# Kernel optimization log

Hardware: AMD Instinct MI355X
Metric: run time of the kernel (lower is better)

## Reference

```python
import jax, jax.numpy as jnp
import numpy as np

HEADS = 8
OUT_C = 8
NEG_SLOPE = 0.2  # PyG GATConv default


def setup_inputs() -> dict:
    key = jax.random.key(0)
    k = jax.random.split(key, 6)
    N, F, E = 100000, 128, 1600000
    x = jax.random.normal(k[0], (N, F), dtype=jnp.float32)
    edge_index = jax.random.randint(k[1], (2, E), 0, N, dtype=jnp.int64)
    W = jax.random.normal(k[2], (F, HEADS * OUT_C), dtype=jnp.float32) * (1.0 / np.sqrt(F))
    att_src = jax.random.normal(k[3], (HEADS, OUT_C), dtype=jnp.float32) * 0.1
    att_dst = jax.random.normal(k[4], (HEADS, OUT_C), dtype=jnp.float32) * 0.1
    bias = jnp.zeros((HEADS * OUT_C,), dtype=jnp.float32)
    return {"x": x, "edge_index": edge_index, "W": W,
            "att_src": att_src, "att_dst": att_dst, "bias": bias}


def reference(x, edge_index, W, att_src, att_dst, bias):
    N = x.shape[0]
    # add self loops (PyG default add_self_loops=True)
    loops = jnp.arange(N, dtype=edge_index.dtype)
    src = jnp.concatenate([edge_index[0], loops])  # [E']
    dst = jnp.concatenate([edge_index[1], loops])  # [E']

    h = (x @ W).reshape(N, HEADS, OUT_C)          # [N,H,C]
    a_src = jnp.einsum('nhc,hc->nh', h, att_src)  # [N,H]
    a_dst = jnp.einsum('nhc,hc->nh', h, att_dst)  # [N,H]

    # per-edge LeakyReLU attention logits
    e = jax.nn.leaky_relu(a_src[src] + a_dst[dst], NEG_SLOPE)  # [E',H]

    # segment softmax over incoming edges of each destination node
    emax = jax.ops.segment_max(e, dst, num_segments=N)  # every node has a self loop
    ex = jnp.exp(e - emax[dst])
    denom = jax.ops.segment_sum(ex, dst, num_segments=N)
    alpha = ex / denom[dst]  # [E',H]  (dropout on alpha skipped: eval mode)

    # scatter-add weighted source features
    out = jax.ops.segment_sum(alpha[:, :, None] * h[src], dst, num_segments=N)  # [N,H,C]
    return out.reshape(N, HEADS * OUT_C) + bias
```

## Files before the change

### kernel.cpp

```cpp
#include <hip/hip_runtime.h>
#include <hip/hip_bf16.h>


#define F 128
#define HC 64
#define H 8
#define NS 32
#define PB 512

__device__ inline ushort f2bf(float f) {
    unsigned u = __float_as_uint(f);
    u += 0x7fff + ((u >> 16) & 1);
    return (ushort)(u >> 16);
}

__global__ __launch_bounds__(256) void k_gemm(const float* __restrict__ x,
                                              const float* __restrict__ W,
                                              const float* __restrict__ att_src,
                                              const float* __restrict__ att_dst,
                                              ushort* __restrict__ h2,
                                              float* __restrict__ a_src,
                                              float* __restrict__ a_dst, int N) {
    __shared__ float xs[64][F];
    const int tid  = threadIdx.x;
    const int row0 = blockIdx.x * 64;
    #pragma unroll
    for (int i = 0; i < 8; ++i) {
        int idx = i * 256 + tid;
        int r = idx >> 5;
        float4 v = make_float4(0.f, 0.f, 0.f, 0.f);
        if (row0 + r < N) v = ((const float4*)x)[(size_t)row0 * 32 + idx];
        ((float4*)xs)[idx] = v;
    }
    __syncthreads();
    const int c0 = (tid & 15) * 4;
    const int r0 = (tid >> 4) * 4;
    float acc[4][4] = {};
    for (int k = 0; k < F; k += 4) {
        float w[4][4];
        *(float4*)w[0] = *(const float4*)&W[(size_t)(k + 0) * HC + c0];
        *(float4*)w[1] = *(const float4*)&W[(size_t)(k + 1) * HC + c0];
        *(float4*)w[2] = *(const float4*)&W[(size_t)(k + 2) * HC + c0];
        *(float4*)w[3] = *(const float4*)&W[(size_t)(k + 3) * HC + c0];
        #pragma unroll
        for (int i = 0; i < 4; ++i) {
            float4 xv = *(const float4*)&xs[r0 + i][k];
            #pragma unroll
            for (int c = 0; c < 4; ++c) {
                acc[i][c] += xv.x * w[0][c];
                acc[i][c] += xv.y * w[1][c];
                acc[i][c] += xv.z * w[2][c];
                acc[i][c] += xv.w * w[3][c];
            }
        }
    }
    const int head = (tid & 15) >> 1;
    const int cb   = c0 & 7;
    float as4[4], ad4[4];
    #pragma unroll
    for (int c = 0; c < 4; ++c) {
        as4[c] = att_src[head * 8 + cb + c];
        ad4[c] = att_dst[head * 8 + cb + c];
    }
    #pragma unroll
    for (int i = 0; i < 4; ++i) {
        int r = row0 + r0 + i;
        if (r < N) {
            ushort4 pk;
            pk.x = f2bf(acc[i][0]); pk.y = f2bf(acc[i][1]);
            pk.z = f2bf(acc[i][2]); pk.w = f2bf(acc[i][3]);
            *(ushort4*)&h2[(size_t)r * HC + c0] = pk;
            float ps = acc[i][0]*as4[0] + acc[i][1]*as4[1] +
                       acc[i][2]*as4[2] + acc[i][3]*as4[3];
            float pd = acc[i][0]*ad4[0] + acc[i][1]*ad4[1] +
                       acc[i][2]*ad4[2] + acc[i][3]*ad4[3];
            ps += __shfl_xor(ps, 1);
            pd += __shfl_xor(pd, 1);
            if ((tid & 1) == 0) {
                a_src[(size_t)r * H + head] = ps;
                a_dst[(size_t)r * H + head] = pd;
            }
        }
    }
}

__device__ inline unsigned grp_of(int d, unsigned Mg) {
    return (unsigned)(((unsigned long long)(unsigned)d * Mg) >> 32);
}

__global__ __launch_bounds__(256) void k_c(const int* __restrict__ ei,
                                           int* __restrict__ pcntT,
                                           int E, unsigned Mg) {
    __shared__ int cnt[8];
    if (threadIdx.x < 8) cnt[threadIdx.x] = 0;
    __syncthreads();
    const int t    = blockIdx.x * 256 + threadIdx.x;
    const int nthr = PB * 256;
    const int a0 = (4 - (E & 3)) & 3;
    const int nv = (E - a0) >> 2;
    const int4* vd = (const int4*)(ei + E + a0);
    for (int q = t; q < nv; q += nthr) {
        int4 d = vd[q];
        atomicAdd(&cnt[grp_of(d.x, Mg)], 1);
        atomicAdd(&cnt[grp_of(d.y, Mg)], 1);
        atomicAdd(&cnt[grp_of(d.z, Mg)], 1);
        atomicAdd(&cnt[grp_of(d.w, Mg)], 1);
    }
    if (blockIdx.x == 0) {
        int r = (E - a0) & 3;
        int e = -1;
        int tx = (int)threadIdx.x;
        if (tx < a0) e = tx;
        else if (tx - a0 < r) e = a0 + (nv << 2) + (tx - a0);
        if (e >= 0) atomicAdd(&cnt[grp_of(ei[E + e], Mg)], 1);
    }
    __syncthreads();
    if (threadIdx.x < 8) pcntT[(size_t)threadIdx.x * PB + blockIdx.x] = cnt[threadIdx.x];
}

__global__ __launch_bounds__(1024) void k_sA(int* __restrict__ pcntT,
                                             int* __restrict__ gEdgeBase, int E) {
    __shared__ int s[1024];
    const int S2 = 8 * PB;
    const int base = threadIdx.x * (S2 / 1024);
    int v[4]; int sum = 0;
    #pragma unroll
    for (int k = 0; k < S2 / 1024; ++k) { v[k] = pcntT[base + k]; sum += v[k]; }
    s[threadIdx.x] = sum;
    __syncthreads();
    for (int d = 1; d < 1024; d <<= 1) {
        int t = (threadIdx.x >= d) ? s[threadIdx.x - d] : 0;
        __syncthreads();
        s[threadIdx.x] += t;
        __syncthreads();
    }
    int run = s[threadIdx.x] - sum;
    #pragma unroll
    for (int k = 0; k < S2 / 1024; ++k) {
        int idx = base + k;
        pcntT[idx] = run;
        if ((idx % PB) == 0) gEdgeBase[idx / PB] = run;
        run += v[k];
    }
    if (threadIdx.x == 0) gEdgeBase[8] = E;
}

__global__ __launch_bounds__(256) void k_p(const int* __restrict__ ei,
                                           const int* __restrict__ pcntT,
                                           unsigned* __restrict__ payload,
                                           int E, unsigned Mg, int npg) {
    __shared__ int lpos[8];
    if (threadIdx.x < 8) lpos[threadIdx.x] = pcntT[(size_t)threadIdx.x * PB + blockIdx.x];
    __syncthreads();
    const int t    = blockIdx.x * 256 + threadIdx.x;
    const int nthr = PB * 256;
    const int a0 = (4 - (E & 3)) & 3;
    const int nv = (E - a0) >> 2;
    const int4* vd = (const int4*)(ei + E + a0);
    for (int q = t; q < nv; q += nthr) {
        int4 d = vd[q];
        int e = a0 + (q << 2);
        int s0 = ei[e], s1 = ei[e + 1], s2 = ei[e + 2], s3 = ei[e + 3];
        unsigned g; int pos;
        g = grp_of(d.x, Mg); pos = atomicAdd(&lpos[g], 1);
        payload[pos] = ((unsigned)s0 << 14) | (unsigned)(d.x - (int)g * npg);
        g = grp_of(d.y, Mg); pos = atomicAdd(&lpos[g], 1);
        payload[pos] = ((unsigned)s1 << 14) | (unsigned)(d.y - (int)g * npg);
        g = grp_of(d.z, Mg); pos = atomicAdd(&lpos[g], 1);
        payload[pos] = ((unsigned)s2 << 14) | (unsigned)(d.z - (int)g * npg);
        g = grp_of(d.w, Mg); pos = atomicAdd(&lpos[g], 1);
        payload[pos] = ((unsigned)s3 << 14) | (unsigned)(d.w - (int)g * npg);
    }
    if (blockIdx.x == 0) {
        int r = (E - a0) & 3;
        int e = -1;
        int tx = (int)threadIdx.x;
        if (tx < a0) e = tx;
        else if (tx - a0 < r) e = a0 + (nv << 2) + (tx - a0);
        if (e >= 0) {
            int dv = ei[E + e];
            unsigned g = grp_of(dv, Mg);
            int pos = atomicAdd(&lpos[g], 1);
            payload[pos] = ((unsigned)ei[e] << 14) | (unsigned)(dv - (int)g * npg);
        }
    }
}

__global__ __launch_bounds__(1024) void k_h2(const unsigned* __restrict__ payload,
                                             const int* __restrict__ gEdgeBase,
                                             ushort* __restrict__ hist, int npg) {
    extern __shared__ int lcnt[];
    const int g = blockIdx.x & 7, sl = blockIdx.x >> 3;
    for (int i = threadIdx.x; i < npg; i += 1024) lcnt[i] = 0;
    __syncthreads();
    const int gb0 = gEdgeBase[g], gb1 = gEdgeBase[g + 1];
    const int chunk = (gb1 - gb0 + NS - 1) / NS;
    const int lo = gb0 + sl * chunk;
    const int hi = min(lo + chunk, gb1);
    for (int i = lo + threadIdx.x; i < hi; i += 1024)
        atomicAdd(&lcnt[payload[i] & 16383u], 1);
    __syncthreads();
    ushort* hrow = hist + (size_t)blockIdx.x * npg;
    for (int i = threadIdx.x; i < npg; i += 1024) hrow[i] = (ushort)lcnt[i];
}

__global__ __launch_bounds__(256) void k_scan1(const ushort* __restrict__ hist,
                                               int* __restrict__ offs,
                                               int* __restrict__ bsums,
                                               int N, int npg) {
    __shared__ int s[256];
    int i = blockIdx.x * 256 + threadIdx.x;
    int v = 0;
    if (i < N) {
        int g = i / npg;
        int c = i - g * npg;
        const ushort* hp = hist + (size_t)g * npg + c;
        #pragma unroll 8
        for (int j = 0; j < NS; ++j) v += hp[(size_t)(j << 3) * npg];
        v += 1;
    }
    s[threadIdx.x] = v;
    __syncthreads();
    for (int d = 1; d < 256; d <<= 1) {
        int t = (threadIdx.x >= d) ? s[threadIdx.x - d] : 0;
        __syncthreads();
        s[threadIdx.x] += t;
        __syncthreads();
    }
    if (i < N) offs[i] = s[threadIdx.x] - v;
    if (threadIdx.x == 255) bsums[blockIdx.x] = s[255];
}

__global__ __launch_bounds__(512) void k_scan2(int* __restrict__ bsums, int nb) {
    __shared__ int s[512];
    int v = (threadIdx.x < nb) ? bsums[threadIdx.x] : 0;
    s[threadIdx.x] = v;
    __syncthreads();
    for (int d = 1; d < 512; d <<= 1) {
        int t = (threadIdx.x >= d) ? s[threadIdx.x - d] : 0;
        __syncthreads();
        s[threadIdx.x] += t;
        __syncthreads();
    }
    if (threadIdx.x < nb) bsums[threadIdx.x] = s[threadIdx.x] - v;
}

__global__ __launch_bounds__(256) void k_scan3(int* __restrict__ offs,
                                               const int* __restrict__ bsums,
                                               ushort* __restrict__ hist,
                                               int* __restrict__ srcs,
                                               int N, int npg, int Etot) {
    int i = blockIdx.x * 256 + threadIdx.x;
    if (i == 0) offs[N] = Etot;
    if (i >= N) return;
    int o = offs[i] + bsums[i >> 8];
    offs[i] = o;
    srcs[o] = i;
    int g = i / npg;
    int c = i - g * npg;
    ushort* hp = hist + (size_t)g * npg + c;
    int p = 0;
    #pragma unroll 8
    for (int j = 0; j < NS; ++j) {
        size_t off = (size_t)(j << 3) * npg;
        int t = hp[off];
        hp[off] = (ushort)p;
        p += t;
    }
}

__global__ __launch_bounds__(1024) void k_scat2(const unsigned* __restrict__ payload,
                                                const int* __restrict__ gEdgeBase,
                                                const ushort* __restrict__ hist,
                                                const int* __restrict__ offs,
                                                int* __restrict__ srcs,
                                                int npg, int N) {
    extern __shared__ int lpos[];
    const int g = blockIdx.x & 7, sl = blockIdx.x >> 3;
    const int lod = g * npg;
    const int len = min(npg, N - lod);
    const ushort* hrow = hist + (size_t)blockIdx.x * npg;
    for (int i = threadIdx.x; i < len; i += 1024)
        lpos[i] = offs[lod + i] + 1 + (int)hrow[i];
    __syncthreads();
    const int gb0 = gEdgeBase[g], gb1 = gEdgeBase[g + 1];
    const int chunk = (gb1 - gb0 + NS - 1) / NS;
    const int lo = gb0 + sl * chunk;
    const int hi = min(lo + chunk, gb1);
    for (int i = lo + threadIdx.x; i < hi; i += 1024) {
        unsigned p = payload[i];
        int pos = atomicAdd(&lpos[p & 16383u], 1);
        srcs[pos] = (int)(p >> 14);
    }
}

__global__ __launch_bounds__(256) void k_gat(const int* __restrict__ offs,
                                             const int* __restrict__ srcs,
                                             const ushort* __restrict__ h2,
                                             const float* __restrict__ a_src,
                                             const float* __restrict__ a_dst,
                                             const float* __restrict__ bias,
                                             float* __restrict__ out, int N) {
    const int lane = threadIdx.x & 63;
    const int half = lane >> 5;
    const int l32  = lane & 31;
    const int g    = l32 >> 3;
    const int hd   = l32 & 7;
    const int wave = threadIdx.x >> 6;
    const int d = blockIdx.x * 8 + wave * 2 + half;
    const bool valid = d < N;

    int off = 0, end = 0;
    float adst = 0.f;
    if (valid) {
        off  = offs[d];
        end  = offs[d + 1];
        adst = a_dst[d * H + hd];
    }

    float acc[8] = {0.f, 0.f, 0.f, 0.f, 0.f, 0.f, 0.f, 0.f};
    float den = 0.f;

    for (int i = off + g; i < end; i += 8) {
        const int i2 = i + 4;
        const bool has1 = (i2 < end);
        int s0 = srcs[i];
        int s1 = has1 ? srcs[i2] : s0;
        float a0 = a_src[s0 * H + hd] + adst;
        float a1 = a_src[s1 * H + hd] + adst;
        a0 = a0 > 0.f ? a0 : 0.2f * a0;
        a1 = a1 > 0.f ? a1 : 0.2f * a1;
        float ex0 = __expf(a0);
        float ex1 = has1 ? __expf(a1) : 0.f;
        uint4 u0 = *(const uint4*)(h2 + ((size_t)s0 << 6) + (hd << 3));
        uint4 u1 = *(const uint4*)(h2 + ((size_t)s1 << 6) + (hd << 3));
        acc[0] += ex0 * __uint_as_float(u0.x << 16);
        acc[1] += ex0 * __uint_as_float(u0.x & 0xffff0000u);
        acc[2] += ex0 * __uint_as_float(u0.y << 16);
        acc[3] += ex0 * __uint_as_float(u0.y & 0xffff0000u);
        acc[4] += ex0 * __uint_as_float(u0.z << 16);
        acc[5] += ex0 * __uint_as_float(u0.z & 0xffff0000u);
        acc[6] += ex0 * __uint_as_float(u0.w << 16);
        acc[7] += ex0 * __uint_as_float(u0.w & 0xffff0000u);
        acc[0] += ex1 * __uint_as_float(u1.x << 16);
        acc[1] += ex1 * __uint_as_float(u1.x & 0xffff0000u);
        acc[2] += ex1 * __uint_as_float(u1.y << 16);
        acc[3] += ex1 * __uint_as_float(u1.y & 0xffff0000u);
        acc[4] += ex1 * __uint_as_float(u1.z << 16);
        acc[5] += ex1 * __uint_as_float(u1.z & 0xffff0000u);
        acc[6] += ex1 * __uint_as_float(u1.w << 16);
        acc[7] += ex1 * __uint_as_float(u1.w & 0xffff0000u);
        den += ex0 + ex1;
    }

    #pragma unroll
    for (int m = 8; m <= 16; m <<= 1) {
        #pragma unroll
        for (int c = 0; c < 8; ++c) acc[c] += __shfl_xor(acc[c], m);
        den += __shfl_xor(den, m);
    }

    if (g == 0 && valid) {
        float r = 1.f / den;
        float4 o0, o1;
        o0.x = acc[0]*r + bias[hd*8+0]; o0.y = acc[1]*r + bias[hd*8+1];
        o0.z = acc[2]*r + bias[hd*8+2]; o0.w = acc[3]*r + bias[hd*8+3];
        o1.x = acc[4]*r + bias[hd*8+4]; o1.y = acc[5]*r + bias[hd*8+5];
        o1.z = acc[6]*r + bias[hd*8+6]; o1.w = acc[7]*r + bias[hd*8+7];
        *(float4*)&out[(size_t)d * HC + hd * 8]     = o0;
        *(float4*)&out[(size_t)d * HC + hd * 8 + 4] = o1;
    }
}

extern "C" void kernel_launch(void* const* d_in, const int* in_sizes, int n_in,
                              void* d_out, int out_size, void* d_ws, size_t ws_size,
                              hipStream_t stream) {
    const float* x       = (const float*)d_in[0];
    const int*   ei      = (const int*)d_in[1];
    const float* W       = (const float*)d_in[2];
    const float* att_src = (const float*)d_in[3];
    const float* att_dst = (const float*)d_in[4];
    const float* bias    = (const float*)d_in[5];
    const int N = in_sizes[0] / F;
    const int E = in_sizes[1] / 2;
    const int Etot = E + N;
    const int npg = (N + 7) / 8;
    const unsigned Mg = (unsigned)(((1ULL << 32) + (unsigned)npg - 1) / (unsigned)npg);
    float* out = (float*)d_out;

    ushort*   h2      = (ushort*)d_ws;
    float*    a_src   = (float*)(h2 + (size_t)N * HC);
    float*    a_dst   = a_src + (size_t)N * H;
    int*      offs    = (int*)(a_dst + (size_t)N * H);
    int*      bsums   = offs + N + 1;
    int*      pcntT   = bsums + 512;
    int*      gEdgeBase = pcntT + 8 * PB;
    ushort*   hist    = (ushort*)(gEdgeBase + 16);
    size_t    histE   = ((size_t)8 * NS * npg + 3) & ~(size_t)3;
    unsigned* payload = (unsigned*)(hist + histE);
    int*      srcs    = (int*)(payload + E);

    const int nb = (N + 255) / 256;
    const size_t ldsz = (size_t)npg * sizeof(int);
    k_gemm <<<(N + 63) / 64, 256, 0, stream>>>(x, W, att_src, att_dst, h2, a_src, a_dst, N);
    k_c    <<<PB, 256, 0, stream>>>(ei, pcntT, E, Mg);
    k_sA   <<<1, 1024, 0, stream>>>(pcntT, gEdgeBase, E);
    k_p    <<<PB, 256, 0, stream>>>(ei, pcntT, payload, E, Mg, npg);
    k_h2   <<<8 * NS, 1024, ldsz, stream>>>(payload, gEdgeBase, hist, npg);
    k_scan1<<<nb, 256, 0, stream>>>(hist, offs, bsums, N, npg);
    k_scan2<<<1, 512, 0, stream>>>(bsums, nb);
    k_scan3<<<nb, 256, 0, stream>>>(offs, bsums, hist, srcs, N, npg, Etot);
    k_scat2<<<8 * NS, 1024, ldsz, stream>>>(payload, gEdgeBase, hist, offs, srcs, npg, N);
    k_gat  <<<(N + 7) / 8, 256, 0, stream>>>(offs, srcs, h2, a_src, a_dst, bias, out, N);
}
```

Baseline: 224.2 us.

## Fuse edge counting into GEMM and merge scan stages into fewer kernels

Moves the per-block destination-group counting into the tail of the GEMM kernel, which runs with more than PB blocks. Each k_p block now redundantly scans the 4096 partial counts itself instead of relying on a separate single-block scan kernel. The three-kernel CSR offset scan is replaced by a reduce kernel plus a kernel that scans the block sums locally and then does the block scan and histogram rewrite. Together these cut the launch count from ten to seven, trading extra redundant scan work per block and extra register use (32 cached histogram values per thread).

Result: faster. 218.3 us (-2.6%).

```diff
diff --git a/kernel.cpp b/kernel.cpp
--- a/kernel.cpp
+++ b/kernel.cpp
@@ -5,6 +5,7 @@
 #define F 128
 #define HC 64
 #define H 8
+#define NG 8
 #define NS 32
 #define PB 512
 
@@ -12,6 +13,10 @@
     unsigned u = __float_as_uint(f);
     u += 0x7fff + ((u >> 16) & 1);
     return (ushort)(u >> 16);
+}
+
+__device__ inline unsigned grp_of(int d, unsigned Mg) {
+    return (unsigned)(((unsigned long long)(unsigned)d * Mg) >> 32);
 }
 
 __global__ __launch_bounds__(256) void k_gemm(const float* __restrict__ x,
@@ -20,8 +25,12 @@
                                               const float* __restrict__ att_dst,
                                               ushort* __restrict__ h2,
                                               float* __restrict__ a_src,
-                                              float* __restrict__ a_dst, int N) {
+                                              float* __restrict__ a_dst,
+                                              const int* __restrict__ ei,
+                                              int* __restrict__ pcntT,
+                                              int N, int E, unsigned Mg) {
     __shared__ float xs[64][F];
+    __shared__ int cnt8[8];
     const int tid  = threadIdx.x;
     const int row0 = blockIdx.x * 64;
     #pragma unroll
@@ -82,106 +91,92 @@
             }
         }
     }
-}
-
-__device__ inline unsigned grp_of(int d, unsigned Mg) {
-    return (unsigned)(((unsigned long long)(unsigned)d * Mg) >> 32);
-}
-
-__global__ __launch_bounds__(256) void k_c(const int* __restrict__ ei,
-                                           int* __restrict__ pcntT,
-                                           int E, unsigned Mg) {
-    __shared__ int cnt[8];
-    if (threadIdx.x < 8) cnt[threadIdx.x] = 0;
-    __syncthreads();
-    const int t    = blockIdx.x * 256 + threadIdx.x;
-    const int nthr = PB * 256;
+
+    if (blockIdx.x < PB) {
+        if (tid < 8) cnt8[tid] = 0;
+        __syncthreads();
+        const int a0 = (4 - (E & 3)) & 3;
+        const int nv = (E - a0) >> 2;
+        const int4* vd = (const int4*)(ei + E + a0);
+        for (int q = blockIdx.x * 256 + tid; q < nv; q += PB * 256) {
+            int4 d = vd[q];
+            atomicAdd(&cnt8[grp_of(d.x, Mg)], 1);
+            atomicAdd(&cnt8[grp_of(d.y, Mg)], 1);
+            atomicAdd(&cnt8[grp_of(d.z, Mg)], 1);
+            atomicAdd(&cnt8[grp_of(d.w, Mg)], 1);
+        }
+        if (blockIdx.x == 0) {
+            int r = (E - a0) & 3;
+            int e = -1;
+            if (tid < a0) e = tid;
+            else if (tid - a0 < r) e = a0 + (nv << 2) + (tid - a0);
+            if (e >= 0) atomicAdd(&cnt8[grp_of(ei[E + e], Mg)], 1);
+        }
+        __syncthreads();
+        if (tid < 8) pcntT[tid * PB + blockIdx.x] = cnt8[tid];
+    }
+}
+
+__global__ __launch_bounds__(256) void k_p(const int* __restrict__ ei,
+                                           const int* __restrict__ pcntT,
+                                           unsigned* __restrict__ payload,
+                                           int* __restrict__ gEdgeBase,
+                                           int E, unsigned Mg, int npg) {
+    __shared__ int sc[NG * PB];
+    __shared__ int sp[256];
+    __shared__ int cur[8];
+    const int tid = threadIdx.x;
+    for (int i = tid; i < NG * PB; i += 256) sc[i] = pcntT[i];
+    __syncthreads();
+    const int b16 = tid * 16;
+    int tmp[16]; int ssum = 0;
+    #pragma unroll
+    for (int k = 0; k < 16; ++k) { tmp[k] = sc[b16 + k]; ssum += tmp[k]; }
+    sp[tid] = ssum;
+    __syncthreads();
+    for (int d = 1; d < 256; d <<= 1) {
+        int t2 = (tid >= d) ? sp[tid - d] : 0;
+        __syncthreads();
+        sp[tid] += t2;
+        __syncthreads();
+    }
+    int run = sp[tid] - ssum;
+    #pragma unroll
+    for (int k = 0; k < 16; ++k) { sc[b16 + k] = run; run += tmp[k]; }
+    __syncthreads();
+    if (tid < 8) cur[tid] = sc[tid * PB + blockIdx.x];
+    if (blockIdx.x == 0) {
+        if (tid < 8) gEdgeBase[tid] = sc[tid * PB];
+        if (tid == 8) gEdgeBase[8] = E;
+    }
+    __syncthreads();
     const int a0 = (4 - (E & 3)) & 3;
     const int nv = (E - a0) >> 2;
     const int4* vd = (const int4*)(ei + E + a0);
-    for (int q = t; q < nv; q += nthr) {
+    for (int q = blockIdx.x * 256 + tid; q < nv; q += PB * 256) {
         int4 d = vd[q];
-        atomicAdd(&cnt[grp_of(d.x, Mg)], 1);
-        atomicAdd(&cnt[grp_of(d.y, Mg)], 1);
-        atomicAdd(&cnt[grp_of(d.z, Mg)], 1);
-        atomicAdd(&cnt[grp_of(d.w, Mg)], 1);
+        int e = a0 + (q << 2);
+        int s0 = ei[e], s1 = ei[e + 1], s2 = ei[e + 2], s3 = ei[e + 3];
+        unsigned gg; int pos;
+        gg = grp_of(d.x, Mg); pos = atomicAdd(&cur[gg], 1);
+        payload[pos] = ((unsigned)s0 << 14) | (unsigned)(d.x - (int)gg * npg);
+        gg = grp_of(d.y, Mg); pos = atomicAdd(&cur[gg], 1);
+        payload[pos] = ((unsigned)s1 << 14) | (unsigned)(d.y - (int)gg * npg);
+        gg = grp_of(d.z, Mg); pos = atomicAdd(&cur[gg], 1);
+        payload[pos] = ((unsigned)s2 << 14) | (unsigned)(d.z - (int)gg * npg);
+        gg = grp_of(d.w, Mg); pos = atomicAdd(&cur[gg], 1);
+        payload[pos] = ((unsigned)s3 << 14) | (unsigned)(d.w - (int)gg * npg);
     }
     if (blockIdx.x == 0) {
         int r = (E - a0) & 3;
         int e = -1;
-        int tx = (int)threadIdx.x;
-        if (tx < a0) e = tx;
-        else if (tx - a0 < r) e = a0 + (nv << 2) + (tx - a0);
-        if (e >= 0) atomicAdd(&cnt[grp_of(ei[E + e], Mg)], 1);
-    }
-    __syncthreads();
-    if (threadIdx.x < 8) pcntT[(size_t)threadIdx.x * PB + blockIdx.x] = cnt[threadIdx.x];
-}
-
-__global__ __launch_bounds__(1024) void k_sA(int* __restrict__ pcntT,
-                                             int* __restrict__ gEdgeBase, int E) {
-    __shared__ int s[1024];
-    const int S2 = 8 * PB;
-    const int base = threadIdx.x * (S2 / 1024);
-    int v[4]; int sum = 0;
-    #pragma unroll
-    for (int k = 0; k < S2 / 1024; ++k) { v[k] = pcntT[base + k]; sum += v[k]; }
-    s[threadIdx.x] = sum;
-    __syncthreads();
-    for (int d = 1; d < 1024; d <<= 1) {
-        int t = (threadIdx.x >= d) ? s[threadIdx.x - d] : 0;
-        __syncthreads();
-        s[threadIdx.x] += t;
-        __syncthreads();
-    }
-    int run = s[threadIdx.x] - sum;
-    #pragma unroll
-    for (int k = 0; k < S2 / 1024; ++k) {
-        int idx = base + k;
-        pcntT[idx] = run;
-        if ((idx % PB) == 0) gEdgeBase[idx / PB] = run;
-        run += v[k];
-    }
-    if (threadIdx.x == 0) gEdgeBase[8] = E;
-}
-
-__global__ __launch_bounds__(256) void k_p(const int* __restrict__ ei,
-                                           const int* __restrict__ pcntT,
-                                           unsigned* __restrict__ payload,
-                                           int E, unsigned Mg, int npg) {
-    __shared__ int lpos[8];
-    if (threadIdx.x < 8) lpos[threadIdx.x] = pcntT[(size_t)threadIdx.x * PB + blockIdx.x];
-    __syncthreads();
-    const int t    = blockIdx.x * 256 + threadIdx.x;
-    const int nthr = PB * 256;
-    const int a0 = (4 - (E & 3)) & 3;
-    const int nv = (E - a0) >> 2;
-    const int4* vd = (const int4*)(ei + E + a0);
-    for (int q = t; q < nv; q += nthr) {
-        int4 d = vd[q];
-        int e = a0 + (q << 2);
-        int s0 = ei[e], s1 = ei[e + 1], s2 = ei[e + 2], s3 = ei[e + 3];
-        unsigned g; int pos;
-        g = grp_of(d.x, Mg); pos = atomicAdd(&lpos[g], 1);
-        payload[pos] = ((unsigned)s0 << 14) | (unsigned)(d.x - (int)g * npg);
-        g = grp_of(d.y, Mg); pos = atomicAdd(&lpos[g], 1);
-        payload[pos] = ((unsigned)s1 << 14) | (unsigned)(d.y - (int)g * npg);
-        g = grp_of(d.z, Mg); pos = atomicAdd(&lpos[g], 1);
-        payload[pos] = ((unsigned)s2 << 14) | (unsigned)(d.z - (int)g * npg);
-        g = grp_of(d.w, Mg); pos = atomicAdd(&lpos[g], 1);
-        payload[pos] = ((unsigned)s3 << 14) | (unsigned)(d.w - (int)g * npg);
-    }
-    if (blockIdx.x == 0) {
-        int r = (E - a0) & 3;
-        int e = -1;
-        int tx = (int)threadIdx.x;
-        if (tx < a0) e = tx;
-        else if (tx - a0 < r) e = a0 + (nv << 2) + (tx - a0);
+        if (tid < a0) e = tid;
+        else if (tid - a0 < r) e = a0 + (nv << 2) + (tid - a0);
         if (e >= 0) {
             int dv = ei[E + e];
-            unsigned g = grp_of(dv, Mg);
-            int pos = atomicAdd(&lpos[g], 1);
-            payload[pos] = ((unsigned)ei[e] << 14) | (unsigned)(dv - (int)g * npg);
+            unsigned gg = grp_of(dv, Mg);
+            int pos = atomicAdd(&cur[gg], 1);
+            payload[pos] = ((unsigned)ei[e] << 14) | (unsigned)(dv - (int)gg * npg);
         }
     }
 }
@@ -204,68 +199,86 @@
     for (int i = threadIdx.x; i < npg; i += 1024) hrow[i] = (ushort)lcnt[i];
 }
 
-__global__ __launch_bounds__(256) void k_scan1(const ushort* __restrict__ hist,
-                                               int* __restrict__ offs,
-                                               int* __restrict__ bsums,
-                                               int N, int npg) {
-    __shared__ int s[256];
-    int i = blockIdx.x * 256 + threadIdx.x;
+__global__ __launch_bounds__(512) void k_s1(const ushort* __restrict__ hist,
+                                            int* __restrict__ bsums,
+                                            int N, int npg, unsigned Mg) {
+    __shared__ int s[512];
+    const int tid = threadIdx.x;
+    const int i = blockIdx.x * 512 + tid;
     int v = 0;
     if (i < N) {
-        int g = i / npg;
-        int c = i - g * npg;
+        unsigned g = grp_of(i, Mg);
+        int c = i - (int)g * npg;
         const ushort* hp = hist + (size_t)g * npg + c;
-        #pragma unroll 8
+        #pragma unroll
         for (int j = 0; j < NS; ++j) v += hp[(size_t)(j << 3) * npg];
         v += 1;
     }
-    s[threadIdx.x] = v;
-    __syncthreads();
-    for (int d = 1; d < 256; d <<= 1) {
-        int t = (threadIdx.x >= d) ? s[threadIdx.x - d] : 0;
-        __syncthreads();
-        s[threadIdx.x] += t;
-        __syncthreads();
-    }
-    if (i < N) offs[i] = s[threadIdx.x] - v;
-    if (threadIdx.x == 255) bsums[blockIdx.x] = s[255];
-}
-
-__global__ __launch_bounds__(512) void k_scan2(int* __restrict__ bsums, int nb) {
+    s[tid] = v;
+    __syncthreads();
+    for (int d = 256; d; d >>= 1) {
+        if (tid < d) s[tid] += s[tid + d];
+        __syncthreads();
+    }
+    if (tid == 0) bsums[blockIdx.x] = s[0];
+}
+
+__global__ __launch_bounds__(512) void k_s3x(ushort* __restrict__ hist,
+                                             const int* __restrict__ bsums,
+                                             int* __restrict__ offs,
+                                             int* __restrict__ srcs,
+                                             int N, int npg, int Etot,
+                                             unsigned Mg, int nbb) {
+    __shared__ int bs[512];
     __shared__ int s[512];
-    int v = (threadIdx.x < nb) ? bsums[threadIdx.x] : 0;
-    s[threadIdx.x] = v;
+    const int tid = threadIdx.x;
+    int myv = (tid < nbb) ? bsums[tid] : 0;
+    bs[tid] = myv;
     __syncthreads();
     for (int d = 1; d < 512; d <<= 1) {
-        int t = (threadIdx.x >= d) ? s[threadIdx.x - d] : 0;
-        __syncthreads();
-        s[threadIdx.x] += t;
-        __syncthreads();
-    }
-    if (threadIdx.x < nb) bsums[threadIdx.x] = s[threadIdx.x] - v;
-}
-
-__global__ __launch_bounds__(256) void k_scan3(int* __restrict__ offs,
-                                               const int* __restrict__ bsums,
-                                               ushort* __restrict__ hist,
-                                               int* __restrict__ srcs,
-                                               int N, int npg, int Etot) {
-    int i = blockIdx.x * 256 + threadIdx.x;
-    if (i == 0) offs[N] = Etot;
-    if (i >= N) return;
-    int o = offs[i] + bsums[i >> 8];
-    offs[i] = o;
-    srcs[o] = i;
-    int g = i / npg;
-    int c = i - g * npg;
-    ushort* hp = hist + (size_t)g * npg + c;
-    int p = 0;
-    #pragma unroll 8
-    for (int j = 0; j < NS; ++j) {
-        size_t off = (size_t)(j << 3) * npg;
-        int t = hp[off];
-        hp[off] = (ushort)p;
-        p += t;
+        int t2 = (tid >= d) ? bs[tid - d] : 0;
+        __syncthreads();
+        bs[tid] += t2;
+        __syncthreads();
+    }
+    const int base = (blockIdx.x == 0) ? 0 : bs[blockIdx.x - 1];
+
+    const int i = blockIdx.x * 512 + tid;
+    int vals[NS];
+    int v = 0;
+    ushort* hp = nullptr;
+    if (i < N) {
+        unsigned g = grp_of(i, Mg);
+        int c = i - (int)g * npg;
+        hp = hist + (size_t)g * npg + c;
+        #pragma unroll
+        for (int j = 0; j < NS; ++j) {
+            vals[j] = hp[(size_t)(j << 3) * npg];
+            v += vals[j];
+        }
+        v += 1;
+    }
+    s[tid] = v;
+    __syncthreads();
+    for (int d = 1; d < 512; d <<= 1) {
+        int t2 = (tid >= d) ? s[tid - d] : 0;
+        __syncthreads();
+        s[tid] += t2;
+        __syncthreads();
+    }
+    const int lexcl = s[tid] - v;
+    if (i == N - 1) offs[N] = Etot;
+    if (i < N) {
+        int o = base + lexcl;
+        offs[i] = o;
+        srcs[o] = i;
+        int p = 0;
+        #pragma unroll
+        for (int j = 0; j < NS; ++j) {
+            size_t off = (size_t)(j << 3) * npg;
+            hp[off] = (ushort)p;
+            p += vals[j];
+        }
     }
 }
 
@@ -384,32 +397,30 @@
     const int N = in_sizes[0] / F;
     const int E = in_sizes[1] / 2;
     const int Etot = E + N;
-    const int npg = (N + 7) / 8;
+    const int npg = (N + NG - 1) / NG;
     const unsigned Mg = (unsigned)(((1ULL << 32) + (unsigned)npg - 1) / (unsigned)npg);
+    const int nbb = (N + 511) / 512;
     float* out = (float*)d_out;
 
     ushort*   h2      = (ushort*)d_ws;
     float*    a_src   = (float*)(h2 + (size_t)N * HC);
     float*    a_dst   = a_src + (size_t)N * H;
     int*      offs    = (int*)(a_dst + (size_t)N * H);
-    int*      bsums   = offs + N + 1;
-    int*      pcntT   = bsums + 512;
-    int*      gEdgeBase = pcntT + 8 * PB;
-    ushort*   hist    = (ushort*)(gEdgeBase + 16);
-    size_t    histE   = ((size_t)8 * NS * npg + 3) & ~(size_t)3;
+    int*      pcntT   = offs + N + 1;
+    int*      gEdgeBase = pcntT + NG * PB;
+    int*      bsums   = gEdgeBase + 16;
+    ushort*   hist    = (ushort*)(bsums + 512);
+    size_t    histE   = ((size_t)NG * NS * npg + 3) & ~(size_t)3;
     unsigned* payload = (unsigned*)(hist + histE);
     int*      srcs    = (int*)(payload + E);
 
-    const int nb = (N + 255) / 256;
     const size_t ldsz = (size_t)npg * sizeof(int);
-    k_gemm <<<(N + 63) / 64, 256, 0, stream>>>(x, W, att_src, att_dst, h2, a_src, a_dst, N);
-    k_c    <<<PB, 256, 0, stream>>>(ei, pcntT, E, Mg);
-    k_sA   <<<1, 1024, 0, stream>>>(pcntT, gEdgeBase, E);
-    k_p    <<<PB, 256, 0, stream>>>(ei, pcntT, payload, E, Mg, npg);
-    k_h2   <<<8 * NS, 1024, ldsz, stream>>>(payload, gEdgeBase, hist, npg);
-    k_scan1<<<nb, 256, 0, stream>>>(hist, offs, bsums, N, npg);
-    k_scan2<<<1, 512, 0, stream>>>(bsums, nb);
-    k_scan3<<<nb, 256, 0, stream>>>(offs, bsums, hist, srcs, N, npg, Etot);
-    k_scat2<<<8 * NS, 1024, ldsz, stream>>>(payload, gEdgeBase, hist, offs, srcs, npg, N);
+    k_gemm <<<(N + 63) / 64, 256, 0, stream>>>(x, W, att_src, att_dst, h2, a_src,
+                                               a_dst, ei, pcntT, N, E, Mg);
+    k_p    <<<PB, 256, 0, stream>>>(ei, pcntT, payload, gEdgeBase, E, Mg, npg);
+    k_h2   <<<NG * NS, 1024, ldsz, stream>>>(payload, gEdgeBase, hist, npg);
+    k_s1   <<<nbb, 512, 0, stream>>>(hist, bsums, N, npg, Mg);
+    k_s3x  <<<nbb, 512, 0, stream>>>(hist, bsums, offs, srcs, N, npg, Etot, Mg, nbb);
+    k_scat2<<<NG * NS, 1024, ldsz, stream>>>(payload, gEdgeBase, hist, offs, srcs, npg, N);
     k_gat  <<<(N + 7) / 8, 256, 0, stream>>>(offs, srcs, h2, a_src, a_dst, bias, out, N);
 }
```
